# Kernel tuning notes

Measured on AMD Instinct MI355X. Metric: run time of the kernel, lower is better.

Reference implementation:

```python
import jax, jax.numpy as jnp
import numpy as np

SEG_LEN = 64
SIG_LEN = 1056
NUM_SEG = 32
STEP = 32  # segment_length * (1 - overlap)

# flat scatter indices: position of element j of segment i in the output signal
_IDX = (np.arange(NUM_SEG)[:, None] * STEP + np.arange(SEG_LEN)[None, :]).reshape(-1)


def combine_segments(segments):
    # segments: (B, C, NUM_SEG, SEG_LEN) -> (B, C, SIG_LEN) overlap-add then normalize
    B, C = segments.shape[0], segments.shape[1]
    idx = jnp.asarray(_IDX)
    out = jnp.zeros((B, C, SIG_LEN), segments.dtype).at[:, :, idx].add(
        segments.reshape(B, C, NUM_SEG * SEG_LEN))
    counter = jnp.zeros((SIG_LEN,), segments.dtype).at[idx].add(1.0)
    return out / counter  # broadcast over (B, C)


def setup_inputs() -> dict:
    key = jax.random.key(0)
    ks = jax.random.split(key, 9)
    B, C, T, E, H = 1024, 8, 32, 128, 256
    s = lambda k, shape, fan: jax.random.normal(k, shape, jnp.float32) * (1.0 / np.sqrt(fan))
    return {
        "encoder_output": jax.random.normal(ks[0], (B, C, T, E), jnp.float32),
        "W1": s(ks[1], (H, E), E), "b1": s(ks[2], (H,), E),
        "W2": s(ks[3], (E, H), H), "b2": s(ks[4], (E,), H),
        "Winv": s(ks[5], (SEG_LEN, E), E), "binv": s(ks[6], (SEG_LEN,), E),
        "Wconv": s(ks[7], (1, C, 3), C * 3), "bconv": s(ks[8], (1,), C * 3),
    }


def reference(encoder_output, W1, b1, W2, b2, Winv, binv, Wconv, bconv):
    # MLP: Linear -> ReLU -> Linear over embedding dim
    h = jax.nn.relu(jnp.einsum('bcte,he->bcth', encoder_output, W1) + b1)
    x = jnp.einsum('bcth,eh->bcte', h, W2) + b2
    # inverse token embedding: E -> SEG_LEN
    x = jnp.einsum('bcte,se->bcts', x, Winv) + binv  # (B, C, T, SEG_LEN)
    # overlap-add reconstruction + normalization
    x = combine_segments(x)  # (B, C, SIG_LEN)
    # ChannelMerger: Conv1d(C -> 1, k=3, padding=1)
    y = jax.lax.conv_general_dilated(
        x, Wconv, window_strides=(1,), padding=[(1, 1)],
        dimension_numbers=('NCH', 'OIH', 'NCH'))
    return y + bconv[None, :, None]
```

## Files before the change

kernel.cpp:

```cpp
#include <hip/hip_runtime.h>
#include <hip/hip_bf16.h>


typedef __bf16 bf16x8 __attribute__((ext_vector_type(8)));
typedef float  f32x4  __attribute__((ext_vector_type(4)));
typedef unsigned int u32;
typedef u32 u32x2 __attribute__((ext_vector_type(2)));

#define L_W1   0
#define L_HS   65536
#define L_SGA  102400
#define L_SGB  119424
#define L_B1   136448
#define L_BC   137472
#define L_WV   137728
#define LDS_SZ 137856

#define BAR_LDS() do {                                              \
    __builtin_amdgcn_sched_barrier(0);                              \
    asm volatile("s_waitcnt lgkmcnt(0)" ::: "memory");              \
    __builtin_amdgcn_s_barrier();                                   \
    __builtin_amdgcn_sched_barrier(0);                              \
  } while (0)

static __device__ __forceinline__ bf16x8 cvt8(f32x4 a, f32x4 b) {
  bf16x8 r;
  r[0] = (__bf16)a[0]; r[1] = (__bf16)a[1]; r[2] = (__bf16)a[2]; r[3] = (__bf16)a[3];
  r[4] = (__bf16)b[0]; r[5] = (__bf16)b[1]; r[6] = (__bf16)b[2]; r[7] = (__bf16)b[3];
  return r;
}
static __device__ __forceinline__ u32 packbf2(float a, float b) {
  union { __hip_bfloat16 h; unsigned short s; } ua, ub;
  ua.h = __float2bfloat16(a); ub.h = __float2bfloat16(b);
  return (u32)ua.s | ((u32)ub.s << 16);
}
static __device__ __forceinline__ float lo16f(u32 w) { return __uint_as_float(w << 16); }
static __device__ __forceinline__ float hi16f(u32 w) { return __uint_as_float(w & 0xffff0000u); }

__global__ __launch_bounds__(256) void k_precomp(
    const float* __restrict__ W2, const float* __restrict__ b2,
    const float* __restrict__ Winv, const float* __restrict__ binv,
    __hip_bfloat16* __restrict__ Wcpre, float* __restrict__ bc) {
  __shared__ float wrow[128];
  const int s = blockIdx.x, h = threadIdx.x;
  if (h < 128) wrow[h] = Winv[s * 128 + h];
  __syncthreads();
  float acc = 0.f;
  #pragma unroll 8
  for (int e = 0; e < 128; ++e) acc = fmaf(wrow[e], W2[e * 256 + h], acc);
  const int nc = h >> 6, ks2 = (h >> 5) & 1, g = (h >> 3) & 3, j = h & 7;
  const int nt2 = s >> 4, q = s & 15;
  Wcpre[((((nc * 2 + ks2) * 4 + nt2) * 4 + g) * 16 + q) * 8 + j] = __float2bfloat16(acc);
  if (h == 0) {
    float a = binv[s];
    for (int e = 0; e < 128; ++e) a = fmaf(wrow[e], b2[e], a);
    bc[s] = a;
  }
}

__global__ __launch_bounds__(512)
__attribute__((amdgpu_waves_per_eu(2, 2)))
void k_gemm(const float* __restrict__ X,
            const float* __restrict__ W1,
            const float* __restrict__ b1,
            const __hip_bfloat16* __restrict__ Wcpre,
            const float* __restrict__ bcp,
            const float* __restrict__ Wcv,
            const float* __restrict__ bcv,
            float* __restrict__ Out)
{
  extern __shared__ __align__(16) char smem[];
  const int tid = threadIdx.x;
  const int wave = tid >> 6, lane = tid & 63;
  const int q = lane & 15, g = lane >> 4;
  const int c = wave;
  const int b0 = blockIdx.x * 4;

  f32x4 xa[16];
  #define LOADX(bb) do {                                                        \
    _Pragma("unroll")                                                           \
    for (int _mt = 0; _mt < 2; ++_mt) {                                         \
      const float* _s = X + ((size_t)((bb) * 8 + c)) * 4096                     \
                          + (_mt * 16 + q) * 128 + g * 8;                       \
      _Pragma("unroll")                                                         \
      for (int _ks = 0; _ks < 4; ++_ks) {                                       \
        xa[(_mt * 4 + _ks) * 2 + 0] = *reinterpret_cast<const f32x4*>(_s + _ks * 32);     \
        xa[(_mt * 4 + _ks) * 2 + 1] = *reinterpret_cast<const f32x4*>(_s + _ks * 32 + 4); \
      } } } while (0)

  LOADX(b0);

  #pragma unroll
  for (int i = 0; i < 8; ++i) {
    const int p8 = tid + i * 512;
    const int fq = p8 & 15, fg = (p8 >> 4) & 3, fks = (p8 >> 6) & 3;
    const int fnt = (p8 >> 8) & 3, fnc = (p8 >> 10) & 3;
    const float* src = W1 + (fnc * 64 + fnt * 16 + fq) * 128 + fks * 32 + fg * 8;
    *reinterpret_cast<bf16x8*>(smem + L_W1 + p8 * 16) =
        cvt8(*reinterpret_cast<const f32x4*>(src),
             *reinterpret_cast<const f32x4*>(src + 4));
  }
  {
    if (tid < 256)               ((float*)(smem + L_B1))[tid]       = b1[tid];
    if (tid >= 256 && tid < 320) ((float*)(smem + L_BC))[tid - 256] = bcp[tid - 256];
    if (tid >= 320 && tid < 344) ((float*)(smem + L_WV))[tid - 320] = Wcv[tid - 320];
    if (tid == 344)              ((float*)(smem + L_WV))[24]        = bcv[0];
    if (tid >= 384 && tid < 448) {
      const int t = tid - 384, buf = t >> 5, cc = (t & 31) >> 2, k = t & 3;
      *reinterpret_cast<u32*>(
          reinterpret_cast<__hip_bfloat16*>(smem + (buf ? L_SGB : L_SGA))
          + cc * 1064 + 1056 + 2 * k) = 0u;
    }
  }
  BAR_LDS();

  __hip_bfloat16* Hb = reinterpret_cast<__hip_bfloat16*>(smem + L_HS) + wave * 2304;
  const float* smB1 = (const float*)(smem + L_B1);
  const float* smBC = (const float*)(smem + L_BC);
  const float* smWV = (const float*)(smem + L_WV);

  #pragma unroll 1
  for (int it = 0; it < 4; ++it) {
    bf16x8 af[2][4];
    #pragma unroll
    for (int f = 0; f < 8; ++f) af[f >> 2][f & 3] = cvt8(xa[2 * f], xa[2 * f + 1]);
    if (it < 3) LOADX(b0 + it + 1);

    f32x4 acc2[2][4] = {};

    for (int nc = 0; nc < 4; ++nc) {
      f32x4 acc1[2][4] = {};
      #pragma unroll
      for (int ks = 0; ks < 4; ++ks) {
        bf16x8 bw[4];
        #pragma unroll
        for (int nt = 0; nt < 4; ++nt)
          bw[nt] = *reinterpret_cast<const bf16x8*>(
              smem + L_W1 + (((nc * 4 + nt) * 4 + ks) << 10) + lane * 16);
        __builtin_amdgcn_s_setprio(1);
        #pragma unroll
        for (int nt = 0; nt < 4; ++nt) {
          acc1[0][nt] = __builtin_amdgcn_mfma_f32_16x16x32_bf16(bw[nt], af[0][ks], acc1[0][nt], 0, 0, 0);
          acc1[1][nt] = __builtin_amdgcn_mfma_f32_16x16x32_bf16(bw[nt], af[1][ks], acc1[1][nt], 0, 0, 0);
        }
        __builtin_amdgcn_s_setprio(0);
      }
      #pragma unroll
      for (int nt = 0; nt < 4; ++nt) {
        const f32x4 b1q = *reinterpret_cast<const f32x4*>(smB1 + nc * 64 + nt * 16 + 4 * g);
        #pragma unroll
        for (int mt = 0; mt < 2; ++mt) {
          u32x2 w;
          w[0] = packbf2(fmaxf(acc1[mt][nt][0] + b1q[0], 0.f),
                         fmaxf(acc1[mt][nt][1] + b1q[1], 0.f));
          w[1] = packbf2(fmaxf(acc1[mt][nt][2] + b1q[2], 0.f),
                         fmaxf(acc1[mt][nt][3] + b1q[3], 0.f));
          *reinterpret_cast<u32x2*>(Hb + (mt * 16 + q) * 72 + nt * 16 + 4 * g) = w;
        }
      }
      #pragma unroll
      for (int ks2 = 0; ks2 < 2; ++ks2) {
        bf16x8 bh[2];
        #pragma unroll
        for (int mt = 0; mt < 2; ++mt)
          bh[mt] = *reinterpret_cast<const bf16x8*>(Hb + (mt * 16 + q) * 72 + ks2 * 32 + g * 8);
        bf16x8 bw2[4];
        #pragma unroll
        for (int nt2 = 0; nt2 < 4; ++nt2)
          bw2[nt2] = *reinterpret_cast<const bf16x8*>(
              Wcpre + ((nc * 2 + ks2) * 4 + nt2) * 512 + lane * 8);
        __builtin_amdgcn_s_setprio(1);
        #pragma unroll
        for (int nt2 = 0; nt2 < 4; ++nt2) {
          acc2[0][nt2] = __builtin_amdgcn_mfma_f32_16x16x32_bf16(bw2[nt2], bh[0], acc2[0][nt2], 0, 0, 0);
          acc2[1][nt2] = __builtin_amdgcn_mfma_f32_16x16x32_bf16(bw2[nt2], bh[1], acc2[1][nt2], 0, 0, 0);
        }
        __builtin_amdgcn_s_setprio(0);
      }
    }

    __hip_bfloat16* Sl = Hb;
    #pragma unroll
    for (int nt2 = 0; nt2 < 4; ++nt2) {
      const f32x4 bcq = *reinterpret_cast<const f32x4*>(smBC + nt2 * 16 + 4 * g);
      #pragma unroll
      for (int mt = 0; mt < 2; ++mt) {
        u32x2 w;
        w[0] = packbf2(acc2[mt][nt2][0] + bcq[0], acc2[mt][nt2][1] + bcq[1]);
        w[1] = packbf2(acc2[mt][nt2][2] + bcq[2], acc2[mt][nt2][3] + bcq[3]);
        *reinterpret_cast<u32x2*>(Sl + (mt * 16 + q) * 68 + nt2 * 16 + 4 * g) = w;
      }
    }

    {
      __hip_bfloat16* sigc = reinterpret_cast<__hip_bfloat16*>(
          smem + ((it & 1) ? L_SGB : L_SGA)) + c * 1064;
      #pragma unroll
      for (int w = 0; w < 5; ++w) {
        const int u = w * 64 + lane;
        if (u < 264) {
          const int p = 4 * u, t = p >> 5, j = p & 31;
          u32x2 r1 = {0u, 0u}, r2 = {0u, 0u};
          if (t < 32) r1 = *reinterpret_cast<const u32x2*>(Sl + t * 68 + j);
          if (t > 0)  r2 = *reinterpret_cast<const u32x2*>(Sl + (t - 1) * 68 + j + 32);
          const float nrm = (t == 0 || t == 32) ? 1.f : 0.5f;
          u32x2 wv;
          wv[0] = packbf2(nrm * (lo16f(r1[0]) + lo16f(r2[0])),
                          nrm * (hi16f(r1[0]) + hi16f(r2[0])));
          wv[1] = packbf2(nrm * (lo16f(r1[1]) + lo16f(r2[1])),
                          nrm * (hi16f(r1[1]) + hi16f(r2[1])));
          *reinterpret_cast<u32x2*>(sigc + p) = wv;
        }
      }
    }

    if (it & 1) {
      BAR_LDS();
      const float bconv = smWV[24];
      #pragma unroll 1
      for (int rr = 0; rr < 2; ++rr) {
        const int u = tid + rr * 512;
        if (u < 528) {
          const int half = (u >= 264) ? 1 : 0;
          const __hip_bfloat16* sg = reinterpret_cast<const __hip_bfloat16*>(
              smem + (half ? L_SGB : L_SGA));
          const int p0 = (u - half * 264) * 4;
          f32x4 acc = {bconv, bconv, bconv, bconv};
          #pragma unroll
          for (int cc = 0; cc < 8; ++cc) {
            const __hip_bfloat16* row = sg + cc * 1064;
            const u32 wm = (p0 > 0) ? *reinterpret_cast<const u32*>(row + p0 - 2) : 0u;
            const u32x2 wc = *reinterpret_cast<const u32x2*>(row + p0);
            const u32 wr = *reinterpret_cast<const u32*>(row + p0 + 4);
            const float l  = hi16f(wm);
            const float a0 = lo16f(wc[0]), a1 = hi16f(wc[0]);
            const float a2 = lo16f(wc[1]), a3 = hi16f(wc[1]);
            const float r  = lo16f(wr);
            const float w0 = smWV[cc * 3], w1 = smWV[cc * 3 + 1], w2 = smWV[cc * 3 + 2];
            acc[0] = fmaf(w0, l,  fmaf(w1, a0, fmaf(w2, a1, acc[0])));
            acc[1] = fmaf(w0, a0, fmaf(w1, a1, fmaf(w2, a2, acc[1])));
            acc[2] = fmaf(w0, a1, fmaf(w1, a2, fmaf(w2, a3, acc[2])));
            acc[3] = fmaf(w0, a2, fmaf(w1, a3, fmaf(w2, r,  acc[3])));
          }
          *reinterpret_cast<f32x4*>(
              Out + (size_t)(b0 + it - 1 + half) * 1056 + p0) = acc;
        }
      }
      if (it != 3) BAR_LDS();
    }
  }
  #undef LOADX
}

extern "C" void kernel_launch(void* const* d_in, const int* in_sizes, int n_in,
                              void* d_out, int out_size, void* d_ws, size_t ws_size,
                              hipStream_t stream) {
  const float* X    = (const float*)d_in[0];
  const float* W1   = (const float*)d_in[1];
  const float* b1   = (const float*)d_in[2];
  const float* W2   = (const float*)d_in[3];
  const float* b2   = (const float*)d_in[4];
  const float* Winv = (const float*)d_in[5];
  const float* binv = (const float*)d_in[6];
  const float* Wcv  = (const float*)d_in[7];
  const float* bcv  = (const float*)d_in[8];

  __hip_bfloat16* Wcpre = (__hip_bfloat16*)((char*)d_ws + 65536);
  float*          bcp   = (float*)((char*)d_ws + 98304);

  k_precomp<<<64, 256, 0, stream>>>(W2, b2, Winv, binv, Wcpre, bcp);
  k_gemm<<<256, 512, LDS_SZ, stream>>>(X, W1, b1, Wcpre, bcp, Wcv, bcv,
                                       (float*)d_out);
}
```

Baseline: 62.89 us.

## Stage fused W2 weights in LDS, single signal buffer, defer next-batch prefetch

Copies the precomputed fused second-layer weights (Wcpre) into LDS once per block so the inner GEMM reads them from shared memory instead of global memory on every iteration. The double signal buffer is replaced by a single buffer, with the conv epilogue now run every iteration on 264 threads instead of every other iteration. The prefetch of the next input batch is moved from before the GEMM loop to after it, which shortens the live range of the prefetch registers. The cost is a larger LDS footprint, an extra barrier pair per iteration, and less overlap of the global X load with compute.

```diff
diff --git a/kernel.cpp b/kernel.cpp
--- a/kernel.cpp
+++ b/kernel.cpp
@@ -9,12 +9,12 @@
 
 #define L_W1   0
 #define L_HS   65536
-#define L_SGA  102400
-#define L_SGB  119424
-#define L_B1   136448
-#define L_BC   137472
-#define L_WV   137728
-#define LDS_SZ 137856
+#define L_SG   102400
+#define L_WC   119424
+#define L_B1   152192
+#define L_BC   153216
+#define L_WV   153472
+#define LDS_SZ 153600
 
 #define BAR_LDS() do {                                              \
     __builtin_amdgcn_sched_barrier(0);                              \
@@ -100,15 +100,21 @@
         cvt8(*reinterpret_cast<const f32x4*>(src),
              *reinterpret_cast<const f32x4*>(src + 4));
   }
+  #pragma unroll
+  for (int i = 0; i < 4; ++i) {
+    const int e = tid + i * 512;
+    *reinterpret_cast<bf16x8*>(smem + L_WC + e * 16) =
+        *reinterpret_cast<const bf16x8*>(Wcpre + e * 8);
+  }
   {
     if (tid < 256)               ((float*)(smem + L_B1))[tid]       = b1[tid];
     if (tid >= 256 && tid < 320) ((float*)(smem + L_BC))[tid - 256] = bcp[tid - 256];
     if (tid >= 320 && tid < 344) ((float*)(smem + L_WV))[tid - 320] = Wcv[tid - 320];
     if (tid == 344)              ((float*)(smem + L_WV))[24]        = bcv[0];
-    if (tid >= 384 && tid < 448) {
-      const int t = tid - 384, buf = t >> 5, cc = (t & 31) >> 2, k = t & 3;
+    if (tid >= 384 && tid < 416) {
+      const int t = tid - 384, cc = t >> 2, k = t & 3;
       *reinterpret_cast<u32*>(
-          reinterpret_cast<__hip_bfloat16*>(smem + (buf ? L_SGB : L_SGA))
+          reinterpret_cast<__hip_bfloat16*>(smem + L_SG)
           + cc * 1064 + 1056 + 2 * k) = 0u;
     }
   }
@@ -124,10 +130,10 @@
     bf16x8 af[2][4];
     #pragma unroll
     for (int f = 0; f < 8; ++f) af[f >> 2][f & 3] = cvt8(xa[2 * f], xa[2 * f + 1]);
-    if (it < 3) LOADX(b0 + it + 1);
 
     f32x4 acc2[2][4] = {};
 
+    #pragma unroll 1
     for (int nc = 0; nc < 4; ++nc) {
       f32x4 acc1[2][4] = {};
       #pragma unroll
@@ -168,7 +174,7 @@
         #pragma unroll
         for (int nt2 = 0; nt2 < 4; ++nt2)
           bw2[nt2] = *reinterpret_cast<const bf16x8*>(
-              Wcpre + ((nc * 2 + ks2) * 4 + nt2) * 512 + lane * 8);
+              smem + L_WC + (((nc * 2 + ks2) * 4 + nt2) * 512 + lane * 8) * 2);
         __builtin_amdgcn_s_setprio(1);
         #pragma unroll
         for (int nt2 = 0; nt2 < 4; ++nt2) {
@@ -178,6 +184,8 @@
         __builtin_amdgcn_s_setprio(0);
       }
     }
+
+    if (it < 3) LOADX(b0 + it + 1);
 
     __hip_bfloat16* Sl = Hb;
     #pragma unroll
@@ -193,8 +201,7 @@
     }
 
     {
-      __hip_bfloat16* sigc = reinterpret_cast<__hip_bfloat16*>(
-          smem + ((it & 1) ? L_SGB : L_SGA)) + c * 1064;
+      __hip_bfloat16* sigc = reinterpret_cast<__hip_bfloat16*>(smem + L_SG) + c * 1064;
       #pragma unroll
       for (int w = 0; w < 5; ++w) {
         const int u = w * 64 + lane;
@@ -214,37 +221,30 @@
       }
     }
 
-    if (it & 1) {
+    {
       BAR_LDS();
       const float bconv = smWV[24];
-      #pragma unroll 1
-      for (int rr = 0; rr < 2; ++rr) {
-        const int u = tid + rr * 512;
-        if (u < 528) {
-          const int half = (u >= 264) ? 1 : 0;
-          const __hip_bfloat16* sg = reinterpret_cast<const __hip_bfloat16*>(
-              smem + (half ? L_SGB : L_SGA));
-          const int p0 = (u - half * 264) * 4;
-          f32x4 acc = {bconv, bconv, bconv, bconv};
-          #pragma unroll
-          for (int cc = 0; cc < 8; ++cc) {
-            const __hip_bfloat16* row = sg + cc * 1064;
-            const u32 wm = (p0 > 0) ? *reinterpret_cast<const u32*>(row + p0 - 2) : 0u;
-            const u32x2 wc = *reinterpret_cast<const u32x2*>(row + p0);
-            const u32 wr = *reinterpret_cast<const u32*>(row + p0 + 4);
-            const float l  = hi16f(wm);
-            const float a0 = lo16f(wc[0]), a1 = hi16f(wc[0]);
-            const float a2 = lo16f(wc[1]), a3 = hi16f(wc[1]);
-            const float r  = lo16f(wr);
-            const float w0 = smWV[cc * 3], w1 = smWV[cc * 3 + 1], w2 = smWV[cc * 3 + 2];
-            acc[0] = fmaf(w0, l,  fmaf(w1, a0, fmaf(w2, a1, acc[0])));
-            acc[1] = fmaf(w0, a0, fmaf(w1, a1, fmaf(w2, a2, acc[1])));
-            acc[2] = fmaf(w0, a1, fmaf(w1, a2, fmaf(w2, a3, acc[2])));
-            acc[3] = fmaf(w0, a2, fmaf(w1, a3, fmaf(w2, r,  acc[3])));
-          }
-          *reinterpret_cast<f32x4*>(
-              Out + (size_t)(b0 + it - 1 + half) * 1056 + p0) = acc;
-        }
+      if (tid < 264) {
+        const __hip_bfloat16* sg = reinterpret_cast<const __hip_bfloat16*>(smem + L_SG);
+        const int p0 = tid * 4;
+        f32x4 acc = {bconv, bconv, bconv, bconv};
+        #pragma unroll
+        for (int cc = 0; cc < 8; ++cc) {
+          const __hip_bfloat16* row = sg + cc * 1064;
+          const u32 wm = (p0 > 0) ? *reinterpret_cast<const u32*>(row + p0 - 2) : 0u;
+          const u32x2 wc = *reinterpret_cast<const u32x2*>(row + p0);
+          const u32 wr = *reinterpret_cast<const u32*>(row + p0 + 4);
+          const float l  = hi16f(wm);
+          const float a0 = lo16f(wc[0]), a1 = hi16f(wc[0]);
+          const float a2 = lo16f(wc[1]), a3 = hi16f(wc[1]);
+          const float r  = lo16f(wr);
+          const float w0 = smWV[cc * 3], w1 = smWV[cc * 3 + 1], w2 = smWV[cc * 3 + 2];
+          acc[0] = fmaf(w0, l,  fmaf(w1, a0, fmaf(w2, a1, acc[0])));
+          acc[1] = fmaf(w0, a0, fmaf(w1, a1, fmaf(w2, a2, acc[1])));
+          acc[2] = fmaf(w0, a1, fmaf(w1, a2, fmaf(w2, a3, acc[2])));
+          acc[3] = fmaf(w0, a2, fmaf(w1, a3, fmaf(w2, r,  acc[3])));
+        }
+        *reinterpret_cast<f32x4*>(Out + (size_t)(b0 + it) * 1056 + p0) = acc;
       }
       if (it != 3) BAR_LDS();
     }
```

Result: faster. 60.34 us (-4.1%).
